# Performance work log

Measured on AMD Instinct MI355X. Metric: run time of the kernel, lower is better.

Reference implementation:

```python
import jax, jax.numpy as jnp
import numpy as np

D_MODEL = 1024
N_HEAD = 16
D_K = 64
NEG_INF = -1e30

def setup_inputs() -> dict:
    key = jax.random.key(0)
    ks = jax.random.split(key, 10)
    bs, l_x = 4, 2048
    s = 1.0 / np.sqrt(D_MODEL)
    return {
        "x": jax.random.normal(ks[0], (bs, D_MODEL, l_x), dtype=jnp.float32),
        "mask": jax.random.randint(ks[1], (bs, l_x), 0, 2, dtype=jnp.int32),
        "Wq": jax.random.normal(ks[2], (D_MODEL, D_MODEL), dtype=jnp.float32) * s,
        "bq": jnp.zeros((D_MODEL,), dtype=jnp.float32),
        "Wk": jax.random.normal(ks[3], (D_MODEL, D_MODEL), dtype=jnp.float32) * s,
        "bk": jnp.zeros((D_MODEL,), dtype=jnp.float32),
        "Wv": jax.random.normal(ks[4], (D_MODEL, D_MODEL), dtype=jnp.float32) * s,
        "bv": jnp.zeros((D_MODEL,), dtype=jnp.float32),
        "Wf": jax.random.normal(ks[5], (D_MODEL, D_MODEL), dtype=jnp.float32) * s,
        "bf": jnp.zeros((D_MODEL,), dtype=jnp.float32),
    }

def reference(x, mask, Wq, bq, Wk, bk, Wv, bv, Wf, bf):
    # x: [bs, d_model, l_x] -> [bs, l_x, d_model]
    bs, _, l_x = x.shape
    xt = jnp.transpose(x, (0, 2, 1))
    a = 1.0 / np.sqrt(D_K)
    q = (xt @ Wq + bq).reshape(bs, l_x, N_HEAD, D_K)
    k = (xt @ Wk + bk).reshape(bs, l_x, N_HEAD, D_K)
    v = (xt @ Wv + bv).reshape(bs, l_x, N_HEAD, D_K)
    # scores: [bs, n_head, l_q, l_k]
    scores = jnp.einsum('bqhd,bkhd->bhqk', q, k) * a
    m = mask.astype(scores.dtype)[:, None, None, :]  # key padding mask
    scores = scores * m + (1.0 - m) * NEG_INF        # mask_logits
    attn = jax.nn.softmax(scores, axis=-1)           # dropout = identity (eval)
    out = jnp.einsum('bhqk,bkhd->bqhd', attn, v).reshape(bs, l_x, D_MODEL)
    out = out @ Wf + bf
    return jnp.transpose(out, (0, 2, 1))  # [bs, d_model, l_x]
```

## Files before the change

### kernel.cpp

```cpp
#include <hip/hip_runtime.h>

#define D_MODEL 1024
#define NHEAD   16
#define DK      64
#define SEQ     2048
#define BATCH   4
#define MTOT    (BATCH * SEQ)
#define NEG_INF (-1e30f)
#define QSCALE  0.18033688f
#define FIXMAX  6.0f

typedef float    f32x4  __attribute__((ext_vector_type(4)));
typedef float    f32x16 __attribute__((ext_vector_type(16)));
typedef _Float16 half8  __attribute__((ext_vector_type(8)));
typedef unsigned uint4v __attribute__((ext_vector_type(4)));

__device__ __forceinline__ unsigned hb(float f) {
    _Float16 h = (_Float16)f;
    return (unsigned)__builtin_bit_cast(unsigned short, h);
}
__device__ __forceinline__ uint2 pack4h(float a, float b, float c, float d) {
    uint2 r; r.x = hb(a) | (hb(b) << 16); r.y = hb(c) | (hb(d) << 16); return r;
}
__device__ __forceinline__ void plswap(unsigned &a, unsigned &b) {
    typedef int v2i __attribute__((ext_vector_type(2)));
    v2i r = __builtin_amdgcn_permlane32_swap((int)a, (int)b, false, false);
    a = (unsigned)r[0]; b = (unsigned)r[1];
}

__global__ __launch_bounds__(256)
void prep_transpose(const float* __restrict__ x,
                    const float* __restrict__ Wq, const float* __restrict__ Wk,
                    const float* __restrict__ Wv, const float* __restrict__ Wf,
                    _Float16* __restrict__ xt,
                    _Float16* __restrict__ WTq, _Float16* __restrict__ WTk,
                    _Float16* __restrict__ WTv, _Float16* __restrict__ WTf)
{
    __shared__ float tile[64][65];
    const int z = blockIdx.z;
    const float* src; _Float16* dst; int R, C;
    if (z < 4) {
        src = x + (size_t)z * D_MODEL * SEQ;
        dst = xt + (size_t)z * SEQ * D_MODEL;
        R = D_MODEL; C = SEQ;
    } else {
        if (blockIdx.x >= 16) return;
        R = D_MODEL; C = D_MODEL;
        switch (z - 4) {
            case 0: src = Wq; dst = WTq; break;
            case 1: src = Wk; dst = WTk; break;
            case 2: src = Wv; dst = WTv; break;
            default: src = Wf; dst = WTf; break;
        }
    }
    const int r0 = blockIdx.y * 64, c0 = blockIdx.x * 64;
    const int t = threadIdx.x;
#pragma unroll
    for (int it = 0; it < 4; ++it) {
        const int idx = t + it * 256;
        const int lr = idx >> 4, lc = (idx & 15) * 4;
        float4 f = *(const float4*)&src[(long long)(r0 + lr) * C + c0 + lc];
        tile[lr][lc + 0] = f.x; tile[lr][lc + 1] = f.y;
        tile[lr][lc + 2] = f.z; tile[lr][lc + 3] = f.w;
    }
    __syncthreads();
#pragma unroll
    for (int it = 0; it < 2; ++it) {
        const int idx = t + it * 256;
        const int c = idx >> 3, ch = idx & 7;
        uint2 a = pack4h(tile[ch * 8 + 0][c], tile[ch * 8 + 1][c],
                         tile[ch * 8 + 2][c], tile[ch * 8 + 3][c]);
        uint2 b = pack4h(tile[ch * 8 + 4][c], tile[ch * 8 + 5][c],
                         tile[ch * 8 + 6][c], tile[ch * 8 + 7][c]);
        uint4v o; o[0] = a.x; o[1] = a.y; o[2] = b.x; o[3] = b.y;
        *(uint4v*)&dst[(long long)(c0 + c) * R + r0 + ch * 8] = o;
    }
}

__global__ __launch_bounds__(256)
void mask_scan(const int* __restrict__ mask, int* __restrict__ idx,
               int* __restrict__ nkeep)
{
    const int b = blockIdx.x, t = threadIdx.x;
    const int lane = t & 63, w = t >> 6;
    __shared__ int wsum[4];
    __shared__ int base;
    if (t == 0) base = 0;
    __syncthreads();
    for (int c = 0; c < SEQ; c += 256) {
        const int l = c + t;
        const int m = mask[b * SEQ + l];
        unsigned long long bal = __ballot(m != 0);
        int pre = __popcll(bal & ((1ULL << lane) - 1ULL));
        if (lane == 0) wsum[w] = __popcll(bal);
        __syncthreads();
        int off = base;
#pragma unroll
        for (int ww = 0; ww < 4; ++ww) if (ww < w) off += wsum[ww];
        if (m) idx[b * SEQ + off + pre] = l;
        __syncthreads();
        if (t == 0) base += wsum[0] + wsum[1] + wsum[2] + wsum[3];
        __syncthreads();
    }
    if (t == 0) nkeep[b] = base;
}

__global__ __launch_bounds__(256)
void compact_x(const _Float16* __restrict__ xt, const int* __restrict__ idx,
               const int* __restrict__ nkeep, _Float16* __restrict__ xc)
{
    const int b = blockIdx.y, t = threadIdx.x;
    const int j0 = blockIdx.x * 128;
    const int nk = nkeep[b];
    const int nkpad = (nk + 127) & ~127;
    if (j0 >= nkpad) return;
#pragma unroll 1
    for (int p = 0; p < 64; ++p) {
        const int c = t + p * 256;
        const int r = c >> 7;
        const int col = (c & 127) * 8;
        const int j = j0 + r;
        uint4v v = {0u, 0u, 0u, 0u};
        if (j < nk) {
            const int src = idx[b * SEQ + j];
            v = *(const uint4v*)&xt[((long long)b * SEQ + src) * D_MODEL + col];
        }
        *(uint4v*)&xc[((long long)b * SEQ + j) * D_MODEL + col] = v;
    }
}

__global__ __launch_bounds__(256)
void gemm_qkv(const _Float16* __restrict__ xt, const _Float16* __restrict__ xc,
              const _Float16* __restrict__ WTq, const _Float16* __restrict__ WTk,
              const float* __restrict__ bq, const float* __restrict__ bk,
              const float* __restrict__ bv, const int* __restrict__ nkeep,
              _Float16* __restrict__ qh, _Float16* __restrict__ khc,
              _Float16* __restrict__ VTc)
{
    __shared__ __align__(16) _Float16 As[128 * 32];
    __shared__ __align__(16) _Float16 Bs[128 * 32];

    const int t = threadIdx.x, w = t >> 6, l = t & 63;
    const int lo16 = l & 15, hi = l >> 4;
    const int bid = blockIdx.x;

    int bm, bn, mode;
    const _Float16 *Abase, *Bbase;
    if (bid < 512) {
        const int i = (bid & 7) * 64 + (bid >> 3);
        bm = i & 63; bn = i >> 6;
        mode = 0; Abase = xt; Bbase = WTq;
    } else {
        const int b2 = bid - 512;
        const int i = (b2 & 7) * 128 + (b2 >> 3);
        bm = i & 63; bn = i >> 6;
        const int bb = bm >> 4;
        const int j0 = (bm & 15) * 128;
        if (j0 >= ((nkeep[bb] + 127) & ~127)) return;
        mode = (bn < 8) ? 1 : 2;
        Abase = xc; Bbase = WTk;
    }
    const int wr = w >> 1, wc = w & 1;

    f32x4 acc[4][4];
#pragma unroll
    for (int mi = 0; mi < 4; ++mi)
#pragma unroll
        for (int ni = 0; ni < 4; ++ni) acc[mi][ni] = (f32x4){0.f, 0.f, 0.f, 0.f};

    const int srow   = l >> 2;
    const int schunk = (l & 3) ^ ((l >> 3) & 3);
    const _Float16* Ag = Abase + (long long)(bm * 128 + w * 32 + srow) * 1024 + schunk * 8;
    const _Float16* Bg = Bbase + (long long)(bn * 128 + w * 32 + srow) * 1024 + schunk * 8;
    const int ldsOff = (w * 32) * 32;
    const int xr = (lo16 >> 1) & 3;

    for (int k0 = 0; k0 < 1024; k0 += 32) {
        __syncthreads();
        __builtin_amdgcn_global_load_lds(reinterpret_cast<const unsigned int*>(Ag + k0),
                                         reinterpret_cast<unsigned int*>(&As[ldsOff]), 16, 0, 0);
        __builtin_amdgcn_global_load_lds(reinterpret_cast<const unsigned int*>(Ag + k0 + 16 * 1024),
                                         reinterpret_cast<unsigned int*>(&As[ldsOff + 16 * 32]), 16, 0, 0);
        __builtin_amdgcn_global_load_lds(reinterpret_cast<const unsigned int*>(Bg + k0),
                                         reinterpret_cast<unsigned int*>(&Bs[ldsOff]), 16, 0, 0);
        __builtin_amdgcn_global_load_lds(reinterpret_cast<const unsigned int*>(Bg + k0 + 16 * 1024),
                                         reinterpret_cast<unsigned int*>(&Bs[ldsOff + 16 * 32]), 16, 0, 0);
        __syncthreads();

        half8 af[4], bf[4];
#pragma unroll
        for (int mi = 0; mi < 4; ++mi)
            af[mi] = *(const half8*)&As[(wr * 64 + mi * 16 + lo16) * 32 + ((hi ^ xr) << 3)];
#pragma unroll
        for (int ni = 0; ni < 4; ++ni)
            bf[ni] = *(const half8*)&Bs[(wc * 64 + ni * 16 + lo16) * 32 + ((hi ^ xr) << 3)];
#pragma unroll
        for (int mi = 0; mi < 4; ++mi)
#pragma unroll
            for (int ni = 0; ni < 4; ++ni)
                acc[mi][ni] = __builtin_amdgcn_mfma_f32_16x16x32_f16(af[mi], bf[ni], acc[mi][ni], 0, 0, 0);
    }

    if (mode == 0) {
#pragma unroll
        for (int mi = 0; mi < 4; ++mi) {
            const int m = bm * 128 + wr * 64 + mi * 16 + hi * 4;
#pragma unroll
            for (int ni = 0; ni < 4; ++ni) {
                const int n = bn * 128 + wc * 64 + ni * 16 + lo16;
                const float bvv = bq[n];
#pragma unroll
                for (int r = 0; r < 4; ++r)
                    qh[(long long)(m + r) * D_MODEL + n] =
                        (_Float16)((acc[mi][ni][r] + bvv) * QSCALE);
            }
        }
    } else if (mode == 1) {
#pragma unroll
        for (int mi = 0; mi < 4; ++mi) {
            const int m = bm * 128 + wr * 64 + mi * 16 + hi * 4;
#pragma unroll
            for (int ni = 0; ni < 4; ++ni) {
                const int n = bn * 128 + wc * 64 + ni * 16 + lo16;
                const float bvv = bk[n];
#pragma unroll
                for (int r = 0; r < 4; ++r)
                    khc[(long long)(m + r) * D_MODEL + n] = (_Float16)(acc[mi][ni][r] + bvv);
            }
        }
    } else {
        const int bb = bm >> 4;
#pragma unroll
        for (int mi = 0; mi < 4; ++mi) {
            const int m = bm * 128 + wr * 64 + mi * 16 + hi * 4;
            const int j = m & (SEQ - 1);
#pragma unroll
            for (int ni = 0; ni < 4; ++ni) {
                const int nv = bn * 128 + wc * 64 + ni * 16 + lo16 - 1024;
                const float bvv = bv[nv];
                uint2 o = pack4h(acc[mi][ni][0] + bvv, acc[mi][ni][1] + bvv,
                                 acc[mi][ni][2] + bvv, acc[mi][ni][3] + bvv);
                *(uint2*)&VTc[((long long)bb * D_MODEL + nv) * SEQ + j] = o;
            }
        }
    }
}

__global__ __launch_bounds__(256)
void gemm_fin(const _Float16* __restrict__ A, const _Float16* __restrict__ B,
              const float* __restrict__ bias, float* __restrict__ C)
{
    __shared__ __align__(16) _Float16 As[128 * 32];
    __shared__ __align__(16) _Float16 Bs[128 * 32];

    const int t = threadIdx.x, w = t >> 6, l = t & 63;
    const int lo16 = l & 15, hi = l >> 4;
    const int bid = blockIdx.x;
    const int swz = (bid & 7) * 64 + (bid >> 3);
    const int bm = swz & 63, bn = swz >> 6;
    const int wr = w >> 1, wc = w & 1;

    f32x4 acc[4][4];
#pragma unroll
    for (int mi = 0; mi < 4; ++mi)
#pragma unroll
        for (int ni = 0; ni < 4; ++ni) acc[mi][ni] = (f32x4){0.f, 0.f, 0.f, 0.f};

    const int srow   = l >> 2;
    const int schunk = (l & 3) ^ ((l >> 3) & 3);
    const _Float16* Ag = A + (long long)(bm * 128 + w * 32 + srow) * 1024 + schunk * 8;
    const _Float16* Bg = B + (long long)(bn * 128 + w * 32 + srow) * 1024 + schunk * 8;
    const int ldsOff = (w * 32) * 32;
    const int xr = (lo16 >> 1) & 3;

    for (int k0 = 0; k0 < 1024; k0 += 32) {
        __syncthreads();
        __builtin_amdgcn_global_load_lds(reinterpret_cast<const unsigned int*>(Ag + k0),
                                         reinterpret_cast<unsigned int*>(&As[ldsOff]), 16, 0, 0);
        __builtin_amdgcn_global_load_lds(reinterpret_cast<const unsigned int*>(Ag + k0 + 16 * 1024),
                                         reinterpret_cast<unsigned int*>(&As[ldsOff + 16 * 32]), 16, 0, 0);
        __builtin_amdgcn_global_load_lds(reinterpret_cast<const unsigned int*>(Bg + k0),
                                         reinterpret_cast<unsigned int*>(&Bs[ldsOff]), 16, 0, 0);
        __builtin_amdgcn_global_load_lds(reinterpret_cast<const unsigned int*>(Bg + k0 + 16 * 1024),
                                         reinterpret_cast<unsigned int*>(&Bs[ldsOff + 16 * 32]), 16, 0, 0);
        __syncthreads();

        half8 af[4], bf[4];
#pragma unroll
        for (int mi = 0; mi < 4; ++mi)
            af[mi] = *(const half8*)&As[(wr * 64 + mi * 16 + lo16) * 32 + ((hi ^ xr) << 3)];
#pragma unroll
        for (int ni = 0; ni < 4; ++ni)
            bf[ni] = *(const half8*)&Bs[(wc * 64 + ni * 16 + lo16) * 32 + ((hi ^ xr) << 3)];
#pragma unroll
        for (int mi = 0; mi < 4; ++mi)
#pragma unroll
            for (int ni = 0; ni < 4; ++ni)
                acc[mi][ni] = __builtin_amdgcn_mfma_f32_16x16x32_f16(af[mi], bf[ni], acc[mi][ni], 0, 0, 0);
    }

#pragma unroll
    for (int mi = 0; mi < 4; ++mi) {
        const int m  = bm * 128 + wr * 64 + mi * 16 + hi * 4;
        const int bo = m >> 11;
        const int ll = m & (SEQ - 1);
#pragma unroll
        for (int ni = 0; ni < 4; ++ni) {
            const int n = bn * 128 + wc * 64 + ni * 16 + lo16;
            const float bvv = bias[n];
            float4 o;
            o.x = acc[mi][ni][0] + bvv; o.y = acc[mi][ni][1] + bvv;
            o.z = acc[mi][ni][2] + bvv; o.w = acc[mi][ni][3] + bvv;
            *(float4*)&C[((long long)bo * D_MODEL + n) * SEQ + ll] = o;
        }
    }
}

__global__ __launch_bounds__(256)
void attn_mfma(const _Float16* __restrict__ qh, const _Float16* __restrict__ khc,
               const _Float16* __restrict__ VTc, const int* __restrict__ nkeepArr,
               _Float16* __restrict__ attnO)
{
    __shared__ __align__(16) unsigned smem[8192];
    _Float16* ksp = (_Float16*)smem;
    _Float16* vsp = (_Float16*)(smem + 4096);

    const int t = threadIdx.x, w = t >> 6, l = t & 63;
    const int q32 = l & 31;
    const int hi5 = l >> 5;
    const int x7  = q32 & 7;

    const int id = blockIdx.x;
    const int i  = (id & 7) * 128 + (id >> 3);
    const int bh = i >> 4, qb = i & 15;
    const int b = bh >> 4, h = bh & 15;
    const int q0 = qb * 128 + w * 32;

    const int nk = nkeepArr[b];
    const int ntiles = (nk + 63) >> 6;

    const _Float16* kbase = khc + (long long)(b * SEQ) * D_MODEL + h * DK;
    const _Float16* vbase = VTc + ((long long)b * D_MODEL + h * DK) * SEQ;

    half8 qf[4];
#pragma unroll
    for (int kc = 0; kc < 4; ++kc)
        qf[kc] = *(const half8*)&qh[(long long)(b * SEQ + q0 + q32) * D_MODEL
                                    + h * DK + kc * 16 + hi5 * 8];

    f32x16 oacc[2];
    f32x16 sumacc;
#pragma unroll
    for (int j = 0; j < 16; ++j) { oacc[0][j] = 0.f; oacc[1][j] = 0.f; sumacc[j] = 0.f; }

    half8 ones;
#pragma unroll
    for (int j = 0; j < 8; ++j) ones[j] = (_Float16)1.0f;

    const int srr = l >> 3;
    const int scc = (l & 7) ^ srr;

    auto stage = [&](int sel, int kt) {
#pragma unroll
        for (int j = 0; j < 2; ++j) {
            const int row0 = w * 16 + j * 8;
            __builtin_amdgcn_global_load_lds(
                reinterpret_cast<const unsigned int*>(
                    kbase + (long long)(kt * 64 + row0 + srr) * D_MODEL + scc * 8),
                reinterpret_cast<unsigned int*>(ksp + sel * 4096 + row0 * 64), 16, 0, 0);
            __builtin_amdgcn_global_load_lds(
                reinterpret_cast<const unsigned int*>(
                    vbase + (long long)(row0 + srr) * SEQ + kt * 64 + scc * 8),
                reinterpret_cast<unsigned int*>(vsp + sel * 4096 + row0 * 64), 16, 0, 0);
        }
    };

    stage(0, 0);
    __syncthreads();
    int cur = 0;

    for (int kt = 0; kt < ntiles; ++kt) {
        if (kt + 1 < ntiles) stage(cur ^ 1, kt + 1);

        const _Float16* ksc = ksp + cur * 4096;
        const _Float16* vsc = vsp + cur * 4096;
        const bool last = (kt == ntiles - 1) && (nk & 63);

        f32x16 sc[2];
#pragma unroll
        for (int blk = 0; blk < 2; ++blk) {
            if (!last) {
#pragma unroll
                for (int r = 0; r < 16; ++r) sc[blk][r] = -FIXMAX;
            } else {
#pragma unroll
                for (int r = 0; r < 16; ++r) {
                    const int key = kt * 64 + blk * 32 + (r & 3) + 4 * hi5 + 8 * (r >> 2);
                    sc[blk][r] = (key < nk) ? -FIXMAX : NEG_INF;
                }
            }
            __builtin_amdgcn_s_setprio(1);
#pragma unroll
            for (int kc = 0; kc < 4; ++kc) {
                half8 kf = *(const half8*)&ksc[(blk * 32 + q32) * 64
                                               + (((kc * 2 + hi5) ^ x7) << 3)];
                sc[blk] = __builtin_amdgcn_mfma_f32_32x32x16_f16(kf, qf[kc], sc[blk], 0, 0, 0);
            }
            __builtin_amdgcn_s_setprio(0);
        }

#pragma unroll
        for (int blk = 0; blk < 2; ++blk)
#pragma unroll
            for (int r = 0; r < 16; ++r)
                sc[blk][r] = exp2f(sc[blk][r]);

#pragma unroll
        for (int blk = 0; blk < 2; ++blk) {
            unsigned W[8];
#pragma unroll
            for (int i2 = 0; i2 < 8; ++i2) {
                auto pk = __builtin_amdgcn_cvt_pkrtz(sc[blk][2 * i2], sc[blk][2 * i2 + 1]);
                W[i2] = __builtin_bit_cast(unsigned, pk);
            }
            plswap(W[0], W[2]); plswap(W[1], W[3]);
            plswap(W[4], W[6]); plswap(W[5], W[7]);
#pragma unroll
            for (int c = 0; c < 2; ++c) {
                uint4v pw;
                pw[0] = W[c * 4 + 0]; pw[1] = W[c * 4 + 1];
                pw[2] = W[c * 4 + 2]; pw[3] = W[c * 4 + 3];
                half8 pf = __builtin_bit_cast(half8, pw);
                const int kc = blk * 2 + c;
                __builtin_amdgcn_s_setprio(1);
#pragma unroll
                for (int dblk = 0; dblk < 2; ++dblk) {
                    half8 vf = *(const half8*)&vsc[(dblk * 32 + q32) * 64
                                                   + (((kc * 2 + hi5) ^ x7) << 3)];
                    oacc[dblk] = __builtin_amdgcn_mfma_f32_32x32x16_f16(vf, pf, oacc[dblk], 0, 0, 0);
                }
                sumacc = __builtin_amdgcn_mfma_f32_32x32x16_f16(ones, pf, sumacc, 0, 0, 0);
                __builtin_amdgcn_s_setprio(0);
            }
        }

        __syncthreads();
        cur ^= 1;
    }

    float inv = 1.f / sumacc[0];
    unsigned* ob = smem + w * 1152;
#pragma unroll
    for (int dblk = 0; dblk < 2; ++dblk)
#pragma unroll
        for (int i2 = 0; i2 < 8; ++i2) {
            auto pk = __builtin_amdgcn_cvt_pkrtz(oacc[dblk][2 * i2] * inv,
                                                 oacc[dblk][2 * i2 + 1] * inv);
            ob[q32 * 36 + (i2 & 1) + 4 * (i2 >> 1) + 2 * hi5 + 16 * dblk] =
                __builtin_bit_cast(unsigned, pk);
        }
    asm volatile("s_waitcnt lgkmcnt(0)" ::: "memory");
    __builtin_amdgcn_sched_barrier(0);
#pragma unroll
    for (int c = 0; c < 4; ++c) {
        uint4v v4 = *(const uint4v*)&ob[q32 * 36 + hi5 * 16 + c * 4];
        *(uint4v*)&attnO[(long long)(b * SEQ + q0 + q32) * D_MODEL
                         + h * DK + hi5 * 32 + c * 8] = v4;
    }
}

extern "C" void kernel_launch(void* const* d_in, const int* in_sizes, int n_in,
                              void* d_out, int out_size, void* d_ws, size_t ws_size,
                              hipStream_t stream)
{
    const float* x    = (const float*)d_in[0];
    const int*   mask = (const int*)d_in[1];
    const float* Wq   = (const float*)d_in[2];
    const float* bq   = (const float*)d_in[3];
    const float* Wk   = (const float*)d_in[4];
    const float* bk   = (const float*)d_in[5];
    const float* Wv   = (const float*)d_in[6];
    const float* bv   = (const float*)d_in[7];
    const float* Wf   = (const float*)d_in[8];
    const float* bf   = (const float*)d_in[9];
    float* out = (float*)d_out;

    _Float16* xt    = (_Float16*)d_ws;
    _Float16* WTq   = xt    + (size_t)MTOT * D_MODEL;
    _Float16* WTk   = WTq   + (size_t)D_MODEL * D_MODEL;
    _Float16* WTv   = WTk   + (size_t)D_MODEL * D_MODEL;
    _Float16* WTf   = WTv   + (size_t)D_MODEL * D_MODEL;
    _Float16* qh    = WTf   + (size_t)D_MODEL * D_MODEL;
    _Float16* xc    = qh    + (size_t)MTOT * D_MODEL;
    _Float16* khc   = xc    + (size_t)MTOT * D_MODEL;
    _Float16* VTc   = khc   + (size_t)MTOT * D_MODEL;
    _Float16* attnO = VTc   + (size_t)MTOT * D_MODEL;
    int* idxb  = (int*)(attnO + (size_t)MTOT * D_MODEL);
    int* nkeep = idxb + BATCH * SEQ;

    prep_transpose<<<dim3(32, 16, 8), 256, 0, stream>>>(x, Wq, Wk, Wv, Wf,
                                                        xt, WTq, WTk, WTv, WTf);
    mask_scan<<<BATCH, 256, 0, stream>>>(mask, idxb, nkeep);
    compact_x<<<dim3(16, BATCH), 256, 0, stream>>>(xt, idxb, nkeep, xc);

    gemm_qkv<<<1536, 256, 0, stream>>>(xt, xc, WTq, WTk, bq, bk, bv, nkeep,
                                       qh, khc, VTc);

    attn_mfma<<<1024, 256, 0, stream>>>(qh, khc, VTc, nkeep, attnO);

    gemm_fin<<<512, 256, 0, stream>>>(attnO, WTf, bf, out);
}
```

Before: 220.1 us.

## Fuse mask scan into prep kernel and gather K/V rows directly in GEMM

Folds the mask prefix-scan into the transpose/convert kernel as an extra grid slice, and drops the compact_x kernel. The K/V projection GEMM now looks up the kept source row indices and loads from xt directly. This removes two kernel launches and a full write and read of the compacted activation buffer, at the cost of gathered (non-contiguous) row addresses in the GEMM A loads. Padding rows clamp to the last kept index instead of being zero, so the padded K/V outputs hold duplicated values rather than zeros.

```diff
diff --git a/kernel.cpp b/kernel.cpp
--- a/kernel.cpp
+++ b/kernel.cpp
@@ -29,15 +29,46 @@
 }
 
 __global__ __launch_bounds__(256)
-void prep_transpose(const float* __restrict__ x,
-                    const float* __restrict__ Wq, const float* __restrict__ Wk,
-                    const float* __restrict__ Wv, const float* __restrict__ Wf,
-                    _Float16* __restrict__ xt,
-                    _Float16* __restrict__ WTq, _Float16* __restrict__ WTk,
-                    _Float16* __restrict__ WTv, _Float16* __restrict__ WTf)
+void prep_scan(const float* __restrict__ x,
+               const float* __restrict__ Wq, const float* __restrict__ Wk,
+               const float* __restrict__ Wv, const float* __restrict__ Wf,
+               const int* __restrict__ mask,
+               _Float16* __restrict__ xt,
+               _Float16* __restrict__ WTq, _Float16* __restrict__ WTk,
+               _Float16* __restrict__ WTv, _Float16* __restrict__ WTf,
+               int* __restrict__ idx, int* __restrict__ nkeep)
 {
     __shared__ float tile[64][65];
     const int z = blockIdx.z;
+    const int t = threadIdx.x;
+
+    if (z == 8) {
+        if (blockIdx.x != 0 || blockIdx.y >= 4) return;
+        const int b = blockIdx.y;
+        const int lane = t & 63, w = t >> 6;
+        __shared__ int wsum[4];
+        __shared__ int base;
+        if (t == 0) base = 0;
+        __syncthreads();
+        for (int c = 0; c < SEQ; c += 256) {
+            const int l = c + t;
+            const int m = mask[b * SEQ + l];
+            unsigned long long bal = __ballot(m != 0);
+            int pre = __popcll(bal & ((1ULL << lane) - 1ULL));
+            if (lane == 0) wsum[w] = __popcll(bal);
+            __syncthreads();
+            int off = base;
+#pragma unroll
+            for (int ww = 0; ww < 4; ++ww) if (ww < w) off += wsum[ww];
+            if (m) idx[b * SEQ + off + pre] = l;
+            __syncthreads();
+            if (t == 0) base += wsum[0] + wsum[1] + wsum[2] + wsum[3];
+            __syncthreads();
+        }
+        if (t == 0) nkeep[b] = base;
+        return;
+    }
+
     const float* src; _Float16* dst; int R, C;
     if (z < 4) {
         src = x + (size_t)z * D_MODEL * SEQ;
@@ -54,11 +85,10 @@
         }
     }
     const int r0 = blockIdx.y * 64, c0 = blockIdx.x * 64;
-    const int t = threadIdx.x;
 #pragma unroll
     for (int it = 0; it < 4; ++it) {
-        const int idx = t + it * 256;
-        const int lr = idx >> 4, lc = (idx & 15) * 4;
+        const int idx2 = t + it * 256;
+        const int lr = idx2 >> 4, lc = (idx2 & 15) * 4;
         float4 f = *(const float4*)&src[(long long)(r0 + lr) * C + c0 + lc];
         tile[lr][lc + 0] = f.x; tile[lr][lc + 1] = f.y;
         tile[lr][lc + 2] = f.z; tile[lr][lc + 3] = f.w;
@@ -66,8 +96,8 @@
     __syncthreads();
 #pragma unroll
     for (int it = 0; it < 2; ++it) {
-        const int idx = t + it * 256;
-        const int c = idx >> 3, ch = idx & 7;
+        const int idx2 = t + it * 256;
+        const int c = idx2 >> 3, ch = idx2 & 7;
         uint2 a = pack4h(tile[ch * 8 + 0][c], tile[ch * 8 + 1][c],
                          tile[ch * 8 + 2][c], tile[ch * 8 + 3][c]);
         uint2 b = pack4h(tile[ch * 8 + 4][c], tile[ch * 8 + 5][c],
@@ -78,62 +108,11 @@
 }
 
 __global__ __launch_bounds__(256)
-void mask_scan(const int* __restrict__ mask, int* __restrict__ idx,
-               int* __restrict__ nkeep)
-{
-    const int b = blockIdx.x, t = threadIdx.x;
-    const int lane = t & 63, w = t >> 6;
-    __shared__ int wsum[4];
-    __shared__ int base;
-    if (t == 0) base = 0;
-    __syncthreads();
-    for (int c = 0; c < SEQ; c += 256) {
-        const int l = c + t;
-        const int m = mask[b * SEQ + l];
-        unsigned long long bal = __ballot(m != 0);
-        int pre = __popcll(bal & ((1ULL << lane) - 1ULL));
-        if (lane == 0) wsum[w] = __popcll(bal);
-        __syncthreads();
-        int off = base;
-#pragma unroll
-        for (int ww = 0; ww < 4; ++ww) if (ww < w) off += wsum[ww];
-        if (m) idx[b * SEQ + off + pre] = l;
-        __syncthreads();
-        if (t == 0) base += wsum[0] + wsum[1] + wsum[2] + wsum[3];
-        __syncthreads();
-    }
-    if (t == 0) nkeep[b] = base;
-}
-
-__global__ __launch_bounds__(256)
-void compact_x(const _Float16* __restrict__ xt, const int* __restrict__ idx,
-               const int* __restrict__ nkeep, _Float16* __restrict__ xc)
-{
-    const int b = blockIdx.y, t = threadIdx.x;
-    const int j0 = blockIdx.x * 128;
-    const int nk = nkeep[b];
-    const int nkpad = (nk + 127) & ~127;
-    if (j0 >= nkpad) return;
-#pragma unroll 1
-    for (int p = 0; p < 64; ++p) {
-        const int c = t + p * 256;
-        const int r = c >> 7;
-        const int col = (c & 127) * 8;
-        const int j = j0 + r;
-        uint4v v = {0u, 0u, 0u, 0u};
-        if (j < nk) {
-            const int src = idx[b * SEQ + j];
-            v = *(const uint4v*)&xt[((long long)b * SEQ + src) * D_MODEL + col];
-        }
-        *(uint4v*)&xc[((long long)b * SEQ + j) * D_MODEL + col] = v;
-    }
-}
-
-__global__ __launch_bounds__(256)
-void gemm_qkv(const _Float16* __restrict__ xt, const _Float16* __restrict__ xc,
+void gemm_qkv(const _Float16* __restrict__ xt,
               const _Float16* __restrict__ WTq, const _Float16* __restrict__ WTk,
               const float* __restrict__ bq, const float* __restrict__ bk,
               const float* __restrict__ bv, const int* __restrict__ nkeep,
+              const int* __restrict__ idxb,
               _Float16* __restrict__ qh, _Float16* __restrict__ khc,
               _Float16* __restrict__ VTc)
 {
@@ -144,21 +123,32 @@
     const int lo16 = l & 15, hi = l >> 4;
     const int bid = blockIdx.x;
 
+    const int srow   = l >> 2;
+    const int schunk = (l & 3) ^ ((l >> 3) & 3);
+
     int bm, bn, mode;
-    const _Float16 *Abase, *Bbase;
+    const _Float16 *Bbase, *Ag0, *Ag1;
     if (bid < 512) {
         const int i = (bid & 7) * 64 + (bid >> 3);
         bm = i & 63; bn = i >> 6;
-        mode = 0; Abase = xt; Bbase = WTq;
+        mode = 0; Bbase = WTq;
+        Ag0 = xt + (long long)(bm * 128 + w * 32 + srow) * 1024 + schunk * 8;
+        Ag1 = Ag0 + 16 * 1024;
     } else {
         const int b2 = bid - 512;
         const int i = (b2 & 7) * 128 + (b2 >> 3);
         bm = i & 63; bn = i >> 6;
         const int bb = bm >> 4;
         const int j0 = (bm & 15) * 128;
-        if (j0 >= ((nkeep[bb] + 127) & ~127)) return;
+        const int nk = nkeep[bb];
+        if (j0 >= ((nk + 127) & ~127)) return;
         mode = (bn < 8) ? 1 : 2;
-        Abase = xc; Bbase = WTk;
+        Bbase = WTk;
+        const int jr = j0 + w * 32 + srow;
+        const int s0 = idxb[bb * SEQ + min(jr, nk - 1)];
+        const int s1 = idxb[bb * SEQ + min(jr + 16, nk - 1)];
+        Ag0 = xt + ((long long)(bb * SEQ + s0)) * 1024 + schunk * 8;
+        Ag1 = xt + ((long long)(bb * SEQ + s1)) * 1024 + schunk * 8;
     }
     const int wr = w >> 1, wc = w & 1;
 
@@ -168,18 +158,15 @@
 #pragma unroll
         for (int ni = 0; ni < 4; ++ni) acc[mi][ni] = (f32x4){0.f, 0.f, 0.f, 0.f};
 
-    const int srow   = l >> 2;
-    const int schunk = (l & 3) ^ ((l >> 3) & 3);
-    const _Float16* Ag = Abase + (long long)(bm * 128 + w * 32 + srow) * 1024 + schunk * 8;
     const _Float16* Bg = Bbase + (long long)(bn * 128 + w * 32 + srow) * 1024 + schunk * 8;
     const int ldsOff = (w * 32) * 32;
     const int xr = (lo16 >> 1) & 3;
 
     for (int k0 = 0; k0 < 1024; k0 += 32) {
         __syncthreads();
-        __builtin_amdgcn_global_load_lds(reinterpret_cast<const unsigned int*>(Ag + k0),
+        __builtin_amdgcn_global_load_lds(reinterpret_cast<const unsigned int*>(Ag0 + k0),
                                          reinterpret_cast<unsigned int*>(&As[ldsOff]), 16, 0, 0);
-        __builtin_amdgcn_global_load_lds(reinterpret_cast<const unsigned int*>(Ag + k0 + 16 * 1024),
+        __builtin_amdgcn_global_load_lds(reinterpret_cast<const unsigned int*>(Ag1 + k0),
                                          reinterpret_cast<unsigned int*>(&As[ldsOff + 16 * 32]), 16, 0, 0);
         __builtin_amdgcn_global_load_lds(reinterpret_cast<const unsigned int*>(Bg + k0),
                                          reinterpret_cast<unsigned int*>(&Bs[ldsOff]), 16, 0, 0);
@@ -491,19 +478,17 @@
     _Float16* WTv   = WTk   + (size_t)D_MODEL * D_MODEL;
     _Float16* WTf   = WTv   + (size_t)D_MODEL * D_MODEL;
     _Float16* qh    = WTf   + (size_t)D_MODEL * D_MODEL;
-    _Float16* xc    = qh    + (size_t)MTOT * D_MODEL;
-    _Float16* khc   = xc    + (size_t)MTOT * D_MODEL;
+    _Float16* khc   = qh    + (size_t)MTOT * D_MODEL;
     _Float16* VTc   = khc   + (size_t)MTOT * D_MODEL;
     _Float16* attnO = VTc   + (size_t)MTOT * D_MODEL;
     int* idxb  = (int*)(attnO + (size_t)MTOT * D_MODEL);
     int* nkeep = idxb + BATCH * SEQ;
 
-    prep_transpose<<<dim3(32, 16, 8), 256, 0, stream>>>(x, Wq, Wk, Wv, Wf,
-                                                        xt, WTq, WTk, WTv, WTf);
-    mask_scan<<<BATCH, 256, 0, stream>>>(mask, idxb, nkeep);
-    compact_x<<<dim3(16, BATCH), 256, 0, stream>>>(xt, idxb, nkeep, xc);
-
-    gemm_qkv<<<1536, 256, 0, stream>>>(xt, xc, WTq, WTk, bq, bk, bv, nkeep,
+    prep_scan<<<dim3(32, 16, 9), 256, 0, stream>>>(x, Wq, Wk, Wv, Wf, mask,
+                                                   xt, WTq, WTk, WTv, WTf,
+                                                   idxb, nkeep);
+
+    gemm_qkv<<<1536, 256, 0, stream>>>(xt, WTq, WTk, bq, bk, bv, nkeep, idxb,
                                        qh, khc, VTc);
 
     attn_mfma<<<1024, 256, 0, stream>>>(qh, khc, VTc, nkeep, attnO);
```

Result: faster. 183.6 us (-16.6%).
